# Optimization experiments

Hardware: AMD Instinct MI355X
Metric: run time of the kernel (lower is better)

Reference implementation:

```python
import jax, jax.numpy as jnp
import numpy as np

D_MODEL = 256
NUM_ITERS = 5
REG = 0.1
EPS = 1e-12  # torch F.normalize eps


def setup_inputs() -> dict:
    key = jax.random.key(0)
    k1, k2, k3, k4, k5, k6 = jax.random.split(key, 6)
    B, Nd, Ns, D = 16, 1024, 1024, D_MODEL
    bound = 1.0 / np.sqrt(D)
    return {
        "drone_tokens": jax.random.normal(k1, (B, Nd, D), dtype=jnp.float32),
        "sat_tokens": jax.random.normal(k2, (B, Ns, D), dtype=jnp.float32),
        "Wq": jax.random.uniform(k3, (D, D), jnp.float32, -bound, bound),
        "bq": jax.random.uniform(k4, (D,), jnp.float32, -bound, bound),
        "Wk": jax.random.uniform(k5, (D, D), jnp.float32, -bound, bound),
        "bk": jax.random.uniform(k6, (D,), jnp.float32, -bound, bound),
    }


def _l2_normalize(x):
    # matches torch F.normalize(dim=-1): x / max(||x||, eps)
    n = jnp.linalg.norm(x, axis=-1, keepdims=True)
    return x / jnp.maximum(n, EPS)


def reference(drone_tokens, sat_tokens, Wq, bq, Wk, bk):
    # nn.Linear: x @ W^T + b
    q = _l2_normalize(drone_tokens @ Wq.T + bq)   # [B, Nd, D]
    k = _l2_normalize(sat_tokens @ Wk.T + bk)     # [B, Ns, D]
    cost = 1.0 - jnp.einsum("bnd,bmd->bnm", q, k)  # [B, Nd, Ns]
    M = -cost / REG
    for _ in range(NUM_ITERS):
        M = M - jax.scipy.special.logsumexp(M, axis=2, keepdims=True)
        M = M - jax.scipy.special.logsumexp(M, axis=1, keepdims=True)
    transport_plan = jnp.exp(M)
    ot_cost = jnp.mean(jnp.sum(transport_plan * cost, axis=(1, 2)))
    return transport_plan, ot_cost
```

## Files before the change

### kernel.cpp

```cpp
#include <hip/hip_runtime.h>
#include <hip/hip_bf16.h>

#define BATCH 16
#define NQ    1024
#define DM    256
#define NROWS (BATCH * NQ)
#define RINV  10.0f

typedef float  f32x4 __attribute__((ext_vector_type(4)));
typedef short  s16x8 __attribute__((ext_vector_type(8)));

static __device__ __forceinline__ ushort f2bf(float f) {
    unsigned u = __builtin_bit_cast(unsigned, f);
    u += 0x7fffu + ((u >> 16) & 1u);
    return (ushort)(u >> 16);
}
static __device__ __forceinline__ float bf2f(ushort h) {
    return __builtin_bit_cast(float, ((unsigned)h) << 16);
}


__global__ void __launch_bounds__(256) k_prep(const float* __restrict__ Wq,
                                              const float* __restrict__ Wk,
                                              ushort* __restrict__ wp0,
                                              ushort* __restrict__ wp1) {
    int gid = blockIdx.x * 256 + threadIdx.x;
    const float* Wsrc = (gid < 8192) ? Wq : Wk;
    ushort* dst = (gid < 8192) ? wp0 : wp1;
    int gx = gid & 8191;
    int gcol = gx >> 9, kk = (gx >> 6) & 7, ln = gx & 63;
    const float* srow = Wsrc + (size_t)(gcol * 16 + (ln & 15)) * DM
                             + kk * 32 + (ln >> 4) * 8;
    ushort* d = dst + (size_t)gx * 8;
#pragma unroll
    for (int e = 0; e < 8; e++) d[e] = f2bf(srow[e]);
}

__global__ void __launch_bounds__(256) k_proj(
        const float* __restrict__ drone, const float* __restrict__ sat,
        const ushort* __restrict__ wp0, const ushort* __restrict__ wp1,
        const float* __restrict__ bq, const float* __restrict__ bk,
        ushort* __restrict__ qkp) {
    __shared__ union {
        float  As[16][260];
        ushort S[16][280];
    } AB;
    __shared__ float red[4][16];

    int t = threadIdx.x;
    int lane = t & 63, w = t >> 6, l16 = lane & 15, lh = lane >> 4;
    int x = blockIdx.x, xcd = x & 7, j = x >> 3;
    int gbase = (j < 32) ? (xcd * 128 + j * 4)
                         : (1024 + xcd * 128 + (j - 32) * 4);
    const float* xsrc; const ushort* Wp; const float* bias;
    if (gbase < 1024) { xsrc = drone; Wp = wp0; bias = bq; }
    else              { xsrc = sat;   Wp = wp1; bias = bk; }

    s16x8 bvr[8][4];
#pragma unroll
    for (int kk = 0; kk < 8; kk++)
#pragma unroll
        for (int ni = 0; ni < 4; ni++)
            bvr[kk][ni] = *(const s16x8*)(Wp + ((size_t)((w * 4 + ni) * 8 + kk) * 64 + lane) * 8);

    float bcol[4];
#pragma unroll
    for (int ni = 0; ni < 4; ni++) bcol[ni] = bias[w * 64 + ni * 16 + l16];

#pragma unroll
    for (int gi = 0; gi < 4; gi++) {
        int g = gbase + gi;
        int rsrc = (g < 1024) ? g * 16 : g * 16 - NROWS;

        {
            int r = t >> 4, c0 = (t & 15) * 4;
            const float* gp = xsrc + (size_t)(rsrc + r) * DM;
#pragma unroll
            for (int jj = 0; jj < 4; jj++)
                *(f32x4*)&AB.As[r][c0 + jj * 64] = *(const f32x4*)(gp + c0 + jj * 64);
        }
        __syncthreads();

        f32x4 acc[4];
#pragma unroll
        for (int ni = 0; ni < 4; ni++) acc[ni] = f32x4{0.f, 0.f, 0.f, 0.f};
#pragma unroll
        for (int kk = 0; kk < 8; kk++) {
            int k0 = kk * 32 + lh * 8;
            f32x4 a0 = *(const f32x4*)&AB.As[l16][k0];
            f32x4 a1 = *(const f32x4*)&AB.As[l16][k0 + 4];
            s16x8 av;
#pragma unroll
            for (int jj = 0; jj < 4; jj++) {
                av[jj]     = (short)f2bf(a0[jj]);
                av[jj + 4] = (short)f2bf(a1[jj]);
            }
#pragma unroll
            for (int ni = 0; ni < 4; ni++)
                acc[ni] = __builtin_amdgcn_mfma_f32_16x16x32_bf16(av, bvr[kk][ni], acc[ni], 0, 0, 0);
        }
        float ssq[4] = {0.f, 0.f, 0.f, 0.f};
#pragma unroll
        for (int ni = 0; ni < 4; ni++) {
#pragma unroll
            for (int r = 0; r < 4; r++) {
                acc[ni][r] += bcol[ni];
                ssq[r] += acc[ni][r] * acc[ni][r];
            }
        }
#pragma unroll
        for (int off = 1; off < 16; off <<= 1)
#pragma unroll
            for (int r = 0; r < 4; r++) ssq[r] += __shfl_xor(ssq[r], off);
        if (l16 == 0)
#pragma unroll
            for (int r = 0; r < 4; r++) red[w][lh * 4 + r] = ssq[r];
        __syncthreads();

        float inv[4];
#pragma unroll
        for (int r = 0; r < 4; r++) {
            int row = lh * 4 + r;
            float tot = red[0][row] + red[1][row] + red[2][row] + red[3][row];
            inv[r] = 1.0f / fmaxf(sqrtf(tot), 1e-12f);
        }
#pragma unroll
        for (int ni = 0; ni < 4; ni++)
#pragma unroll
            for (int r = 0; r < 4; r++)
                AB.S[lh * 4 + r][w * 64 + ni * 16 + l16] = f2bf(acc[ni][r] * inv[r]);
        __syncthreads();
#pragma unroll
        for (int h = 0; h < 2; h++) {
            int kk = w + h * 4;
            s16x8 vv = *(const s16x8*)&AB.S[l16][kk * 32 + lh * 8];
            *(s16x8*)(qkp + ((size_t)(g * 8 + kk) * 64 + lane) * 8) = vv;
        }
        __syncthreads();
    }
}

__global__ void __launch_bounds__(256) k_cost(const ushort* __restrict__ qkp,
                                              char* __restrict__ ktc, int kstride) {
    int t = threadIdx.x, lane = t & 63, w = t >> 6;
    int l16 = lane & 15, lh = lane >> 4;
    int x = blockIdx.x, xcd = x & 7;
    int tile = xcd * 128 + (x >> 3);
    int b = tile >> 6, ty = (tile >> 3) & 7, tx = tile & 7;
    int rg  = b * 64 + ty * 8 + (w >> 1) * 4;
    int cgp = 1024 + b * 64 + tx * 8 + (w & 1) * 4;
    f32x4 acc[4][4];
#pragma unroll
    for (int i = 0; i < 4; i++)
#pragma unroll
        for (int jj = 0; jj < 4; jj++) acc[i][jj] = f32x4{0.f, 0.f, 0.f, 0.f};
#pragma unroll
    for (int kk = 0; kk < 8; kk++) {
        s16x8 am[4], bn[4];
#pragma unroll
        for (int mi = 0; mi < 4; mi++)
            am[mi] = *(const s16x8*)(qkp + ((size_t)((rg + mi) * 8 + kk) * 64 + lane) * 8);
#pragma unroll
        for (int ni = 0; ni < 4; ni++)
            bn[ni] = *(const s16x8*)(qkp + ((size_t)((cgp + ni) * 8 + kk) * 64 + lane) * 8);
#pragma unroll
        for (int mi = 0; mi < 4; mi++)
#pragma unroll
            for (int ni = 0; ni < 4; ni++)
                acc[mi][ni] = __builtin_amdgcn_mfma_f32_16x16x32_bf16(
                    am[mi], bn[ni], acc[mi][ni], 0, 0, 0);
    }
    int rl = ty * 128 + (w >> 1) * 64, cl = tx * 128 + (w & 1) * 64;
#pragma unroll
    for (int mi = 0; mi < 4; mi++)
#pragma unroll
        for (int r = 0; r < 4; r++) {
            int row = rl + mi * 16 + lh * 4 + r;
            ushort* orow = (ushort*)(ktc + (size_t)(b * NQ + row) * (size_t)kstride);
#pragma unroll
            for (int ni = 0; ni < 4; ni++)
                orow[cl + ni * 16 + l16] =
                    f2bf(__expf(fmaf(RINV, acc[mi][ni][r], -RINV)));
        }
}

template<int FIRST>
__global__ void __launch_bounds__(256) k_sink(const char* __restrict__ ktc, int kstride,
                                              const float* __restrict__ partin,
                                              float* __restrict__ u,
                                              float* __restrict__ partout) {
    __shared__ float bsh[NQ];
    __shared__ float pcol[4][NQ];
    int t = threadIdx.x;
    int lane = t & 63, w = t >> 6;
    int x = blockIdx.x;
    int bid = (x & 7) * 64 + (x >> 3);
    int b = bid >> 5, ch = bid & 31;

    if (FIRST) {
        *(f32x4*)&bsh[t * 4] = f32x4{1.f, 1.f, 1.f, 1.f};
    } else {
        f32x4 s = f32x4{0.f, 0.f, 0.f, 0.f};
        const float* pb = partin + (size_t)b * 32 * NQ + t * 4;
#pragma unroll 8
        for (int c = 0; c < 32; c++)
            s += *(const f32x4*)(pb + (size_t)c * NQ);
        f32x4 r;
#pragma unroll
        for (int jj = 0; jj < 4; jj++) r[jj] = 1.0f / s[jj];
        *(f32x4*)&bsh[t * 4] = r;
    }
#pragma unroll
    for (int r = 0; r < 4; r++) *(f32x4*)&pcol[r][t * 4] = f32x4{0.f, 0.f, 0.f, 0.f};
    __syncthreads();

    float br0[8], br1[8];
#pragma unroll
    for (int jj = 0; jj < 8; jj++) {
        br0[jj] = bsh[lane * 8 + jj];
        br1[jj] = bsh[512 + lane * 8 + jj];
    }

    float pa0[8], pa1[8];
#pragma unroll
    for (int jj = 0; jj < 8; jj++) { pa0[jj] = 0.f; pa1[jj] = 0.f; }

    int rowbase = (b << 10) + ch * 32 + w * 8;
#pragma unroll
    for (int rp = 0; rp < 4; rp++) {
        const ushort* ra = (const ushort*)(ktc + (size_t)(rowbase + rp * 2) * (size_t)kstride);
        const ushort* rb = (const ushort*)(ktc + (size_t)(rowbase + rp * 2 + 1) * (size_t)kstride);
        s16x8 ka0 = *(const s16x8*)(ra + lane * 8);
        s16x8 ka1 = *(const s16x8*)(ra + 512 + lane * 8);
        s16x8 kb0 = *(const s16x8*)(rb + lane * 8);
        s16x8 kb1 = *(const s16x8*)(rb + 512 + lane * 8);
        float sa = 0.f, sb = 0.f;
#pragma unroll
        for (int jj = 0; jj < 8; jj++) {
            sa = fmaf(bf2f((ushort)ka0[jj]), br0[jj], sa);
            sa = fmaf(bf2f((ushort)ka1[jj]), br1[jj], sa);
            sb = fmaf(bf2f((ushort)kb0[jj]), br0[jj], sb);
            sb = fmaf(bf2f((ushort)kb1[jj]), br1[jj], sb);
        }
#pragma unroll
        for (int o = 32; o; o >>= 1) {
            sa += __shfl_xor(sa, o);
            sb += __shfl_xor(sb, o);
        }
        float aa = 1.0f / sa, ab = 1.0f / sb;
        if (lane == 0) {
            u[rowbase + rp * 2]     = aa;
            u[rowbase + rp * 2 + 1] = ab;
        }
#pragma unroll
        for (int jj = 0; jj < 8; jj++) {
            pa0[jj] = fmaf(bf2f((ushort)ka0[jj]), aa, pa0[jj]);
            pa0[jj] = fmaf(bf2f((ushort)kb0[jj]), ab, pa0[jj]);
            pa1[jj] = fmaf(bf2f((ushort)ka1[jj]), aa, pa1[jj]);
            pa1[jj] = fmaf(bf2f((ushort)kb1[jj]), ab, pa1[jj]);
        }
    }
#pragma unroll
    for (int jj = 0; jj < 8; jj++) {
        pcol[w][lane * 8 + jj]       = pa0[jj];
        pcol[w][512 + lane * 8 + jj] = pa1[jj];
    }
    __syncthreads();
    {
        f32x4 s = *(const f32x4*)&pcol[0][t * 4];
        s += *(const f32x4*)&pcol[1][t * 4];
        s += *(const f32x4*)&pcol[2][t * 4];
        s += *(const f32x4*)&pcol[3][t * 4];
        *(f32x4*)&partout[((size_t)b * 32 + ch) * NQ + t * 4] = s;
    }
}

__global__ void __launch_bounds__(256) k_final(const char* __restrict__ ktc, int kstride,
                                               const float* __restrict__ partin,
                                               const float* __restrict__ u,
                                               float* __restrict__ out,
                                               float* __restrict__ bprt) {
    __shared__ float bsh[NQ];
    __shared__ float red[4];
    int t = threadIdx.x;
    int lane = t & 63, w = t >> 6;
    int x = blockIdx.x;
    int bid = (x & 7) * 64 + (x >> 3);
    int b = bid >> 5, ch = bid & 31;
    {
        f32x4 s = f32x4{0.f, 0.f, 0.f, 0.f};
        const float* pb = partin + (size_t)b * 32 * NQ + t * 4;
#pragma unroll 8
        for (int c = 0; c < 32; c++)
            s += *(const f32x4*)(pb + (size_t)c * NQ);
        f32x4 r;
#pragma unroll
        for (int jj = 0; jj < 4; jj++) r[jj] = 1.0f / s[jj];
        *(f32x4*)&bsh[t * 4] = r;
    }
    __syncthreads();

    float br0[8], br1[8];
#pragma unroll
    for (int jj = 0; jj < 8; jj++) {
        br0[jj] = bsh[lane * 8 + jj];
        br1[jj] = bsh[512 + lane * 8 + jj];
    }
    float sacc = 0.f;
    int rowbase = (b << 10) + ch * 32 + w * 8;
#pragma unroll
    for (int rr = 0; rr < 8; rr++) {
        int row = rowbase + rr;
        const ushort* kr = (const ushort*)(ktc + (size_t)row * (size_t)kstride);
        s16x8 k0 = *(const s16x8*)(kr + lane * 8);
        s16x8 k1 = *(const s16x8*)(kr + 512 + lane * 8);
        float a = u[row];
        float* orow = out + (size_t)row * NQ;
        float pv0[8], pv1[8];
#pragma unroll
        for (int jj = 0; jj < 8; jj++) {
            float kf0 = bf2f((ushort)k0[jj]);
            float kf1 = bf2f((ushort)k1[jj]);
            float p0 = a * br0[jj] * kf0;
            float p1 = a * br1[jj] * kf1;
            sacc = fmaf(p0, -0.1f * __logf(kf0), sacc);
            sacc = fmaf(p1, -0.1f * __logf(kf1), sacc);
            pv0[jj] = p0; pv1[jj] = p1;
        }
        *(f32x4*)(orow + lane * 8)           = *(f32x4*)&pv0[0];
        *(f32x4*)(orow + lane * 8 + 4)       = *(f32x4*)&pv0[4];
        *(f32x4*)(orow + 512 + lane * 8)     = *(f32x4*)&pv1[0];
        *(f32x4*)(orow + 512 + lane * 8 + 4) = *(f32x4*)&pv1[4];
    }
#pragma unroll
    for (int o = 32; o; o >>= 1) sacc += __shfl_xor(sacc, o);
    if (lane == 0) red[w] = sacc;
    __syncthreads();
    if (t == 0) bprt[blockIdx.x] = red[0] + red[1] + red[2] + red[3];
}

__global__ void k_reduce(const float* __restrict__ bprt, float* __restrict__ out) {
    int t = threadIdx.x;
    float s = bprt[t] + bprt[t + 256];
#pragma unroll
    for (int o = 32; o; o >>= 1) s += __shfl_xor(s, o);
    __shared__ float sm[4];
    if ((t & 63) == 0) sm[t >> 6] = s;
    __syncthreads();
    if (t == 0)
        out[(size_t)BATCH * NQ * NQ] =
            (sm[0] + sm[1] + sm[2] + sm[3]) * (1.0f / BATCH);
}

extern "C" void kernel_launch(void* const* d_in, const int* in_sizes, int n_in,
                              void* d_out, int out_size, void* d_ws, size_t ws_size,
                              hipStream_t stream) {
    const float* drone = (const float*)d_in[0];
    const float* sat   = (const float*)d_in[1];
    const float* Wq    = (const float*)d_in[2];
    const float* bq    = (const float*)d_in[3];
    const float* Wk    = (const float*)d_in[4];
    const float* bk    = (const float*)d_in[5];
    float* out = (float*)d_out;

    char* ws = (char*)d_ws;
    ushort* wp0   = (ushort*)ws;
    ushort* wp1   = (ushort*)(ws + 131072);
    ushort* qkp   = (ushort*)(ws + 262144);
    float*  u     = (float*)(ws + 17039360);
    float*  partA = (float*)(ws + 17104896);
    float*  partB = (float*)(ws + 19202048);
    float*  bprt  = (float*)(ws + 21299200);

    char* ktc; int kstride;
    if (ws_size >= (size_t)54000000) { ktc = ws + 21303296; kstride = 2048; }
    else                             { ktc = (char*)d_out;  kstride = 4096; }

    k_prep<<<64, 256, 0, stream>>>(Wq, Wk, wp0, wp1);
    k_proj<<<512, 256, 0, stream>>>(drone, sat, wp0, wp1, bq, bk, qkp);
    k_cost<<<1024, 256, 0, stream>>>(qkp, ktc, kstride);

    k_sink<1><<<512, 256, 0, stream>>>(ktc, kstride, nullptr, u, partA);
    k_sink<0><<<512, 256, 0, stream>>>(ktc, kstride, partA, u, partB);
    k_sink<0><<<512, 256, 0, stream>>>(ktc, kstride, partB, u, partA);
    k_sink<0><<<512, 256, 0, stream>>>(ktc, kstride, partA, u, partB);
    k_sink<0><<<512, 256, 0, stream>>>(ktc, kstride, partB, u, partA);

    k_final<<<512, 256, 0, stream>>>(ktc, kstride, partA, u, out, bprt);
    k_reduce<<<1, 256, 0, stream>>>(bprt, out);
}
```

Baseline: 113.7 us.

## Split column-partial reduction into separate combine kernel and double Sinkhorn grid

The per-block redundant reduction of column partials (each block summed 32 partial vectors for its batch) is moved into a small k_comb kernel that computes the reciprocal column scale vector once. With that overhead gone, k_sink is relaunched with 1024 blocks, each handling 16 rows instead of 32, producing 64 partials per batch. This cuts redundant partial-sum reads and raises parallelism, at the cost of five extra small kernel launches and a larger partial buffer.

```diff
diff --git a/kernel.cpp b/kernel.cpp
--- a/kernel.cpp
+++ b/kernel.cpp
@@ -184,9 +184,22 @@
         }
 }
 
+__global__ void __launch_bounds__(256) k_comb(const float* __restrict__ part,
+                                              float* __restrict__ bvec) {
+    int blk = blockIdx.x, t = threadIdx.x;
+    int xcd = blk & 7, r = blk >> 3;
+    int batch = 2 * xcd + (r >> 2), quarter = r & 3;
+    int m = quarter * 256 + t;
+    const float* pb = part + (size_t)batch * 64 * NQ + m;
+    float s = 0.f;
+#pragma unroll 8
+    for (int c = 0; c < 64; c++) s += pb[(size_t)c * NQ];
+    bvec[batch * NQ + m] = 1.0f / s;
+}
+
 template<int FIRST>
 __global__ void __launch_bounds__(256) k_sink(const char* __restrict__ ktc, int kstride,
-                                              const float* __restrict__ partin,
+                                              const float* __restrict__ bvec,
                                               float* __restrict__ u,
                                               float* __restrict__ partout) {
     __shared__ float bsh[NQ];
@@ -194,21 +207,13 @@
     int t = threadIdx.x;
     int lane = t & 63, w = t >> 6;
     int x = blockIdx.x;
-    int bid = (x & 7) * 64 + (x >> 3);
-    int b = bid >> 5, ch = bid & 31;
+    int bid = (x & 7) * 128 + (x >> 3);
+    int b = bid >> 6, ch = bid & 63;
 
     if (FIRST) {
         *(f32x4*)&bsh[t * 4] = f32x4{1.f, 1.f, 1.f, 1.f};
     } else {
-        f32x4 s = f32x4{0.f, 0.f, 0.f, 0.f};
-        const float* pb = partin + (size_t)b * 32 * NQ + t * 4;
-#pragma unroll 8
-        for (int c = 0; c < 32; c++)
-            s += *(const f32x4*)(pb + (size_t)c * NQ);
-        f32x4 r;
-#pragma unroll
-        for (int jj = 0; jj < 4; jj++) r[jj] = 1.0f / s[jj];
-        *(f32x4*)&bsh[t * 4] = r;
+        *(f32x4*)&bsh[t * 4] = *(const f32x4*)(bvec + (b << 10) + t * 4);
     }
 #pragma unroll
     for (int r = 0; r < 4; r++) *(f32x4*)&pcol[r][t * 4] = f32x4{0.f, 0.f, 0.f, 0.f};
@@ -225,9 +230,9 @@
 #pragma unroll
     for (int jj = 0; jj < 8; jj++) { pa0[jj] = 0.f; pa1[jj] = 0.f; }
 
-    int rowbase = (b << 10) + ch * 32 + w * 8;
-#pragma unroll
-    for (int rp = 0; rp < 4; rp++) {
+    int rowbase = (b << 10) + ch * 16 + w * 4;
+#pragma unroll
+    for (int rp = 0; rp < 2; rp++) {
         const ushort* ra = (const ushort*)(ktc + (size_t)(rowbase + rp * 2) * (size_t)kstride);
         const ushort* rb = (const ushort*)(ktc + (size_t)(rowbase + rp * 2 + 1) * (size_t)kstride);
         s16x8 ka0 = *(const s16x8*)(ra + lane * 8);
@@ -271,12 +276,12 @@
         s += *(const f32x4*)&pcol[1][t * 4];
         s += *(const f32x4*)&pcol[2][t * 4];
         s += *(const f32x4*)&pcol[3][t * 4];
-        *(f32x4*)&partout[((size_t)b * 32 + ch) * NQ + t * 4] = s;
+        *(f32x4*)&partout[((size_t)b * 64 + ch) * NQ + t * 4] = s;
     }
 }
 
 __global__ void __launch_bounds__(256) k_final(const char* __restrict__ ktc, int kstride,
-                                               const float* __restrict__ partin,
+                                               const float* __restrict__ bvec,
                                                const float* __restrict__ u,
                                                float* __restrict__ out,
                                                float* __restrict__ bprt) {
@@ -287,17 +292,8 @@
     int x = blockIdx.x;
     int bid = (x & 7) * 64 + (x >> 3);
     int b = bid >> 5, ch = bid & 31;
-    {
-        f32x4 s = f32x4{0.f, 0.f, 0.f, 0.f};
-        const float* pb = partin + (size_t)b * 32 * NQ + t * 4;
-#pragma unroll 8
-        for (int c = 0; c < 32; c++)
-            s += *(const f32x4*)(pb + (size_t)c * NQ);
-        f32x4 r;
-#pragma unroll
-        for (int jj = 0; jj < 4; jj++) r[jj] = 1.0f / s[jj];
-        *(f32x4*)&bsh[t * 4] = r;
-    }
+
+    *(f32x4*)&bsh[t * 4] = *(const f32x4*)(bvec + (b << 10) + t * 4);
     __syncthreads();
 
     float br0[8], br1[8];
@@ -368,24 +364,24 @@
     ushort* wp1   = (ushort*)(ws + 131072);
     ushort* qkp   = (ushort*)(ws + 262144);
     float*  u     = (float*)(ws + 17039360);
-    float*  partA = (float*)(ws + 17104896);
-    float*  partB = (float*)(ws + 19202048);
-    float*  bprt  = (float*)(ws + 21299200);
+    float*  bvec  = (float*)(ws + 17104896);
+    float*  part  = (float*)(ws + 17170432);
+    float*  bprt  = (float*)(ws + 21364736);
 
     char* ktc; int kstride;
-    if (ws_size >= (size_t)54000000) { ktc = ws + 21303296; kstride = 2048; }
+    if (ws_size >= (size_t)55000000) { ktc = ws + 21368832; kstride = 2048; }
     else                             { ktc = (char*)d_out;  kstride = 4096; }
 
     k_prep<<<64, 256, 0, stream>>>(Wq, Wk, wp0, wp1);
     k_proj<<<512, 256, 0, stream>>>(drone, sat, wp0, wp1, bq, bk, qkp);
     k_cost<<<1024, 256, 0, stream>>>(qkp, ktc, kstride);
 
-    k_sink<1><<<512, 256, 0, stream>>>(ktc, kstride, nullptr, u, partA);
-    k_sink<0><<<512, 256, 0, stream>>>(ktc, kstride, partA, u, partB);
-    k_sink<0><<<512, 256, 0, stream>>>(ktc, kstride, partB, u, partA);
-    k_sink<0><<<512, 256, 0, stream>>>(ktc, kstride, partA, u, partB);
-    k_sink<0><<<512, 256, 0, stream>>>(ktc, kstride, partB, u, partA);
-
-    k_final<<<512, 256, 0, stream>>>(ktc, kstride, partA, u, out, bprt);
+    k_sink<1><<<1024, 256, 0, stream>>>(ktc, kstride, bvec, u, part);
+    for (int it = 1; it < 5; it++) {
+        k_comb<<<64, 256, 0, stream>>>(part, bvec);
+        k_sink<0><<<1024, 256, 0, stream>>>(ktc, kstride, bvec, u, part);
+    }
+    k_comb<<<64, 256, 0, stream>>>(part, bvec);
+    k_final<<<512, 256, 0, stream>>>(ktc, kstride, bvec, u, out, bprt);
     k_reduce<<<1, 256, 0, stream>>>(bprt, out);
 }
```

Result: slower. 127.0 us (+11.6%).
